# Optimization experiments

Hardware: AMD Instinct MI355X
Metric: run time of the kernel (lower is better)

The kernel has to match this reference:

```python
import jax, jax.numpy as jnp
import numpy as np

N_LOC = 100000
N_EVT = 100000
N_EDGE = 1600000
F_LOC = 128
F_EVT = 128
QID_DIM = 16
QID_BUCKETS = 4096
HID = 64


def setup_inputs() -> dict:
    key = jax.random.key(0)
    ks = jax.random.split(key, 16)
    s = 0.05
    emb = jax.random.normal(ks[4], (QID_BUCKETS + 1, QID_DIM), jnp.float32) * s
    emb = emb.at[0].set(0.0)  # padding_idx=0
    return {
        "loc_feat": jax.random.normal(ks[0], (N_LOC, F_LOC), jnp.float32),
        "evt_feat": jax.random.normal(ks[1], (N_EVT, F_EVT), jnp.float32),
        "qid_bucket": jax.random.randint(ks[2], (N_LOC,), 0, QID_BUCKETS + 1),
        "edge_index": jax.random.randint(ks[3], (2, N_EDGE), 0, N_LOC),
        "emb": emb,
        "W_loc": jax.random.normal(ks[5], (F_LOC + QID_DIM, HID), jnp.float32) * s,
        "b_loc": jnp.zeros((HID,), jnp.float32),
        "W_evt": jax.random.normal(ks[6], (F_EVT, HID), jnp.float32) * s,
        "b_evt": jnp.zeros((HID,), jnp.float32),
        "W_l": jax.random.normal(ks[7], (HID, HID), jnp.float32) * s,
        "b_l": jnp.zeros((HID,), jnp.float32),
        "W_r": jax.random.normal(ks[8], (HID, HID), jnp.float32) * s,
        "W_h1": jax.random.normal(ks[9], (HID, HID // 2), jnp.float32) * s,
        "b_h1": jnp.zeros((HID // 2,), jnp.float32),
        "W_h2": jax.random.normal(ks[10], (HID // 2, 1), jnp.float32) * s,
        "b_h2": jnp.zeros((1,), jnp.float32),
    }


def reference(loc_feat, evt_feat, qid_bucket, edge_index, emb,
              W_loc, b_loc, W_evt, b_evt, W_l, b_l, W_r,
              W_h1, b_h1, W_h2, b_h2):
    # location input = [x || qid_embedding]
    loc_in = jnp.concatenate([loc_feat, emb[qid_bucket]], axis=1)
    loc_x = jax.nn.relu(loc_in @ W_loc + b_loc)          # [N_loc, H]
    evt_x = jax.nn.relu(evt_feat @ W_evt + b_evt)        # [N_evt, H]

    src, dst = edge_index[0], edge_index[1]
    msg = evt_x[src]                                     # [E, H] gather
    summed = jax.ops.segment_sum(msg, dst, num_segments=N_LOC)
    cnt = jax.ops.segment_sum(jnp.ones((msg.shape[0],), msg.dtype), dst,
                              num_segments=N_LOC)
    mean = summed / jnp.maximum(cnt, 1.0)[:, None]       # scatter-mean aggr

    # SAGEConv: lin_l(mean of neighbors) + lin_r(self)
    loc_x = jax.nn.relu(mean @ W_l + b_l + loc_x @ W_r)

    h = jax.nn.relu(loc_x @ W_h1 + b_h1)
    logits = (h @ W_h2 + b_h2)[:, 0]
    return logits
```

## Files before the change

kernel.cpp:

```cpp
#include <hip/hip_runtime.h>

#define N_LOC 100000
#define N_EVT 100000
#define N_EDGE 1600000
#define NB 391
#define NBIN 391
#define BCAPP 9216
#define TILE 4096
#define RBLK 64
#define DGRID 1563

typedef short bf16x8 __attribute__((ext_vector_type(8)));
typedef float f32x4  __attribute__((ext_vector_type(4)));

__device__ __forceinline__ unsigned bf16_rne(float x) {
    unsigned u = __float_as_uint(x);
    return (u + 0x7fffu + ((u >> 16) & 1u)) >> 16;
}
__device__ __forceinline__ float bf_lo(unsigned u) { return __uint_as_float(u << 16); }
__device__ __forceinline__ float bf_hi(unsigned u) { return __uint_as_float(u & 0xffff0000u); }

__device__ __forceinline__ bf16x8 frag_from_f32(const float* p) {
    float4 v0 = *(const float4*)p;
    float4 v1 = *(const float4*)(p + 4);
    uint4 pk = make_uint4(bf16_rne(v0.x) | (bf16_rne(v0.y) << 16),
                          bf16_rne(v0.z) | (bf16_rne(v0.w) << 16),
                          bf16_rne(v1.x) | (bf16_rne(v1.y) << 16),
                          bf16_rne(v1.z) | (bf16_rne(v1.w) << 16));
    return *(bf16x8*)&pk;
}

__global__ __launch_bounds__(256) void k_prep(
    const float* __restrict__ W_evt, const float* __restrict__ W_loc,
    const float* __restrict__ W_l, const float* __restrict__ W_r,
    const float* __restrict__ W_h1,
    unsigned short* __restrict__ Wt_evt,
    unsigned short* __restrict__ Wt_loc,
    unsigned short* __restrict__ Wt_c,
    unsigned short* __restrict__ Wt_h1,
    unsigned* __restrict__ dummy_row)
{
    const int g0 = blockIdx.x * 256 + threadIdx.x;
    const int gs = gridDim.x * 256;
    for (int idx = g0; idx < 64 * 64; idx += gs) {
        int kp = idx >> 6, c = idx & 63;
        *(unsigned*)&Wt_evt[c * 128 + 2 * kp] =
            bf16_rne(W_evt[(2 * kp + 0) * 64 + c]) |
            (bf16_rne(W_evt[(2 * kp + 1) * 64 + c]) << 16);
    }
    for (int idx = g0; idx < 80 * 64; idx += gs) {
        int kp = idx >> 6, c = idx & 63;
        unsigned v = 0;
        if (kp < 72)
            v = bf16_rne(W_loc[(2 * kp + 0) * 64 + c]) |
                (bf16_rne(W_loc[(2 * kp + 1) * 64 + c]) << 16);
        *(unsigned*)&Wt_loc[c * 160 + 2 * kp] = v;
    }
    for (int idx = g0; idx < 64 * 64; idx += gs) {
        int kp = idx >> 6, c = idx & 63;
        float w0, w1;
        if (kp < 32) { w0 = W_l[(2 * kp + 0) * 64 + c]; w1 = W_l[(2 * kp + 1) * 64 + c]; }
        else { w0 = W_r[(2 * kp - 64 + 0) * 64 + c]; w1 = W_r[(2 * kp - 64 + 1) * 64 + c]; }
        *(unsigned*)&Wt_c[c * 128 + 2 * kp] = bf16_rne(w0) | (bf16_rne(w1) << 16);
    }
    for (int idx = g0; idx < 32 * 32; idx += gs) {
        int kp = idx >> 5, c = idx & 31;
        *(unsigned*)&Wt_h1[c * 64 + 2 * kp] =
            bf16_rne(W_h1[(2 * kp + 0) * 32 + c]) |
            (bf16_rne(W_h1[(2 * kp + 1) * 32 + c]) << 16);
    }
    if (blockIdx.x == 0 && threadIdx.x < 32) dummy_row[threadIdx.x] = 0u;
}

__global__ __launch_bounds__(256) void k_front(
    const float* __restrict__ evt_feat, const unsigned short* __restrict__ Wt_evt,
    const float* __restrict__ b_evt, unsigned short* __restrict__ evtb,
    const float* __restrict__ loc_feat, const int* __restrict__ qid,
    const float* __restrict__ emb, const unsigned short* __restrict__ Wt_loc,
    const float* __restrict__ b_loc, unsigned short* __restrict__ locxb,
    const int* __restrict__ ei, int* __restrict__ cntm, int* __restrict__ offm,
    unsigned* __restrict__ binned)
{
    __shared__ int h[NB];
    __shared__ int sh[512];
    const int bid = blockIdx.x;
    const int t = threadIdx.x;

    if (bid < NBIN) {
        for (int i = t; i < NB; i += 256) h[i] = 0;
        __syncthreads();
        const int e0 = bid * TILE;
        int srcv[16], dstv[16], rnk[16];
#pragma unroll
        for (int j = 0; j < 16; ++j) {
            int e = e0 + j * 256 + t;
            if (e < N_EDGE) {
                srcv[j] = ei[e];
                dstv[j] = ei[N_EDGE + e];
                rnk[j] = atomicAdd(&h[dstv[j] >> 8], 1);
            }
        }
        __syncthreads();
        sh[t] = (t < NB) ? h[t] : 0;
        sh[t + 256] = (t + 256 < NB) ? h[t + 256] : 0;
        __syncthreads();
        for (int off = 1; off < 512; off <<= 1) {
            int v0 = (t >= off) ? sh[t - off] : 0;
            int v1 = (t + 256 >= off) ? sh[t + 256 - off] : 0;
            __syncthreads();
            sh[t] += v0;
            sh[t + 256] += v1;
            __syncthreads();
        }
        for (int i = t; i < NB; i += 256) {
            cntm[(size_t)bid * NB + i] = h[i];
            offm[(size_t)bid * NB + i] = sh[i] - h[i];
        }
#pragma unroll
        for (int j = 0; j < 16; ++j) {
            int e = e0 + j * 256 + t;
            if (e < N_EDGE) {
                int bk = dstv[j] >> 8;
                binned[(size_t)bid * TILE + (sh[bk] - h[bk]) + rnk[j]] =
                    (unsigned)srcv[j] | ((unsigned)(dstv[j] & 255) << 24);
            }
        }
        return;
    }

    const int lane = t & 63;
    const int w = t >> 6;
    const int colL = lane & 15;
    const int kq = lane >> 4;

    int db = bid - NBIN;
    if (db < DGRID) {
        const int gbase = db * RBLK;
        const int arow = min(gbase + 16 * w + colL, N_EVT - 1);
        const float* frow = evt_feat + (size_t)arow * 128;
        f32x4 acc0 = {0.f, 0.f, 0.f, 0.f}, acc1 = acc0, acc2 = acc0, acc3 = acc0;
#pragma unroll
        for (int s = 0; s < 4; ++s) {
            const int kb = s * 32 + kq * 8;
            bf16x8 a  = frag_from_f32(frow + kb);
            bf16x8 b0 = *(const bf16x8*)&Wt_evt[(colL +  0) * 128 + kb];
            bf16x8 b1 = *(const bf16x8*)&Wt_evt[(colL + 16) * 128 + kb];
            bf16x8 b2 = *(const bf16x8*)&Wt_evt[(colL + 32) * 128 + kb];
            bf16x8 b3 = *(const bf16x8*)&Wt_evt[(colL + 48) * 128 + kb];
            acc0 = __builtin_amdgcn_mfma_f32_16x16x32_bf16(a, b0, acc0, 0, 0, 0);
            acc1 = __builtin_amdgcn_mfma_f32_16x16x32_bf16(a, b1, acc1, 0, 0, 0);
            acc2 = __builtin_amdgcn_mfma_f32_16x16x32_bf16(a, b2, acc2, 0, 0, 0);
            acc3 = __builtin_amdgcn_mfma_f32_16x16x32_bf16(a, b3, acc3, 0, 0, 0);
        }
        const float bias0 = b_evt[colL +  0];
        const float bias1 = b_evt[colL + 16];
        const float bias2 = b_evt[colL + 32];
        const float bias3 = b_evt[colL + 48];
        const int rbase = gbase + 16 * w + kq * 4;
#pragma unroll
        for (int j = 0; j < 4; ++j) {
            int grow = rbase + j;
            if (grow < N_EVT) {
                size_t o = (size_t)grow * 64;
                evtb[o + colL +  0] = (unsigned short)bf16_rne(fmaxf(acc0[j] + bias0, 0.f));
                evtb[o + colL + 16] = (unsigned short)bf16_rne(fmaxf(acc1[j] + bias1, 0.f));
                evtb[o + colL + 32] = (unsigned short)bf16_rne(fmaxf(acc2[j] + bias2, 0.f));
                evtb[o + colL + 48] = (unsigned short)bf16_rne(fmaxf(acc3[j] + bias3, 0.f));
            }
        }
        return;
    }

    {
        db -= DGRID;
        const int gbase = db * RBLK;
        const int arow = min(gbase + 16 * w + colL, N_LOC - 1);
        const float* frow = loc_feat + (size_t)arow * 128;
        f32x4 acc0 = {0.f, 0.f, 0.f, 0.f}, acc1 = acc0, acc2 = acc0, acc3 = acc0;
#pragma unroll
        for (int s = 0; s < 4; ++s) {
            const int kb = s * 32 + kq * 8;
            bf16x8 a  = frag_from_f32(frow + kb);
            bf16x8 b0 = *(const bf16x8*)&Wt_loc[(colL +  0) * 160 + kb];
            bf16x8 b1 = *(const bf16x8*)&Wt_loc[(colL + 16) * 160 + kb];
            bf16x8 b2 = *(const bf16x8*)&Wt_loc[(colL + 32) * 160 + kb];
            bf16x8 b3 = *(const bf16x8*)&Wt_loc[(colL + 48) * 160 + kb];
            acc0 = __builtin_amdgcn_mfma_f32_16x16x32_bf16(a, b0, acc0, 0, 0, 0);
            acc1 = __builtin_amdgcn_mfma_f32_16x16x32_bf16(a, b1, acc1, 0, 0, 0);
            acc2 = __builtin_amdgcn_mfma_f32_16x16x32_bf16(a, b2, acc2, 0, 0, 0);
            acc3 = __builtin_amdgcn_mfma_f32_16x16x32_bf16(a, b3, acc3, 0, 0, 0);
        }
        {
            const int kb = 128 + kq * 8;
            bf16x8 a;
            if (kq < 2) {
                int q = qid[arow];
                a = frag_from_f32(emb + (size_t)q * 16 + kq * 8);
            } else {
                uint4 z = make_uint4(0, 0, 0, 0);
                a = *(bf16x8*)&z;
            }
            bf16x8 b0 = *(const bf16x8*)&Wt_loc[(colL +  0) * 160 + kb];
            bf16x8 b1 = *(const bf16x8*)&Wt_loc[(colL + 16) * 160 + kb];
            bf16x8 b2 = *(const bf16x8*)&Wt_loc[(colL + 32) * 160 + kb];
            bf16x8 b3 = *(const bf16x8*)&Wt_loc[(colL + 48) * 160 + kb];
            acc0 = __builtin_amdgcn_mfma_f32_16x16x32_bf16(a, b0, acc0, 0, 0, 0);
            acc1 = __builtin_amdgcn_mfma_f32_16x16x32_bf16(a, b1, acc1, 0, 0, 0);
            acc2 = __builtin_amdgcn_mfma_f32_16x16x32_bf16(a, b2, acc2, 0, 0, 0);
            acc3 = __builtin_amdgcn_mfma_f32_16x16x32_bf16(a, b3, acc3, 0, 0, 0);
        }
        const float bias0 = b_loc[colL +  0];
        const float bias1 = b_loc[colL + 16];
        const float bias2 = b_loc[colL + 32];
        const float bias3 = b_loc[colL + 48];
        const int rbase = gbase + 16 * w + kq * 4;
#pragma unroll
        for (int j = 0; j < 4; ++j) {
            int grow = rbase + j;
            if (grow < N_LOC) {
                size_t o = (size_t)grow * 64;
                locxb[o + colL +  0] = (unsigned short)bf16_rne(fmaxf(acc0[j] + bias0, 0.f));
                locxb[o + colL + 16] = (unsigned short)bf16_rne(fmaxf(acc1[j] + bias1, 0.f));
                locxb[o + colL + 32] = (unsigned short)bf16_rne(fmaxf(acc2[j] + bias2, 0.f));
                locxb[o + colL + 48] = (unsigned short)bf16_rne(fmaxf(acc3[j] + bias3, 0.f));
            }
        }
    }
}

__global__ __launch_bounds__(256) void k_bfill(const int* __restrict__ cntm,
                                               const int* __restrict__ offm,
                                               const unsigned* __restrict__ binned,
                                               int* __restrict__ deg,
                                               int* __restrict__ row_ex,
                                               int* __restrict__ csr) {
    __shared__ int cnt0[NBIN];
    __shared__ int off0[NBIN];
    __shared__ int degl[256];
    __shared__ int sc[256];
    __shared__ int cur[256];
    const int b = blockIdx.x;
    const int t = threadIdx.x;
    for (int i = t; i < NBIN; i += 256) {
        cnt0[i] = cntm[(size_t)i * NB + b];
        off0[i] = offm[(size_t)i * NB + b];
    }
    degl[t] = 0;
    __syncthreads();
    for (int blk = t; blk < NBIN; blk += 256) {
        const int c = cnt0[blk];
        const unsigned* s = binned + (size_t)blk * TILE + off0[blk];
        for (int j = 0; j < c; ++j) atomicAdd(&degl[s[j] >> 24], 1);
    }
    __syncthreads();
    const int v = degl[t];
    const int vpad = (v + 15) & ~15;
    sc[t] = vpad;
    __syncthreads();
    for (int off = 1; off < 256; off <<= 1) {
        int x = (t >= off) ? sc[t - off] : 0;
        __syncthreads();
        sc[t] += x;
        __syncthreads();
    }
    const int ex = b * BCAPP + sc[t] - vpad;
    const int loc = b * 256 + t;
    if (loc < N_LOC) { deg[loc] = v; row_ex[loc] = ex; }
    cur[t] = ex;
    __syncthreads();
    for (int blk = t; blk < NBIN; blk += 256) {
        const int c = cnt0[blk];
        const unsigned* s = binned + (size_t)blk * TILE + off0[blk];
        for (int j = 0; j < c; ++j) {
            unsigned u = s[j];
            int pos = atomicAdd(&cur[u >> 24], 1);
            csr[pos] = (int)(u & 0x00FFFFFFu);
        }
    }
    for (int j = v; j < vpad; ++j) csr[ex + j] = N_EVT;
}

__global__ __launch_bounds__(256, 8) void k_aggr(const unsigned* __restrict__ evtb,
                                                 const int* __restrict__ row_ex,
                                                 const int* __restrict__ deg,
                                                 const int* __restrict__ csr,
                                                 unsigned* __restrict__ meanb, int n) {
    const int lane = threadIdx.x & 63;
    int wid = (blockIdx.x * 256 + threadIdx.x) >> 6;
    wid = __builtin_amdgcn_readfirstlane(wid);
    if (wid >= n) return;
    const int beg = row_ex[wid];
    const int cnt = deg[wid];
    const int cntp = (cnt + 15) & ~15;
    const int half = lane >> 5;
    const int c = lane & 31;
    float a0 = 0.0f, a1 = 0.0f;
    for (int i = 0; i < cntp; i += 16) {
        const int bb = beg + i + half;
        int s0 = csr[bb +  0];
        int s1 = csr[bb +  2];
        int s2 = csr[bb +  4];
        int s3 = csr[bb +  6];
        int s4 = csr[bb +  8];
        int s5 = csr[bb + 10];
        int s6 = csr[bb + 12];
        int s7 = csr[bb + 14];
        unsigned u0 = evtb[(size_t)s0 * 32 + c];
        unsigned u1 = evtb[(size_t)s1 * 32 + c];
        unsigned u2 = evtb[(size_t)s2 * 32 + c];
        unsigned u3 = evtb[(size_t)s3 * 32 + c];
        unsigned u4 = evtb[(size_t)s4 * 32 + c];
        unsigned u5 = evtb[(size_t)s5 * 32 + c];
        unsigned u6 = evtb[(size_t)s6 * 32 + c];
        unsigned u7 = evtb[(size_t)s7 * 32 + c];
        a0 += ((bf_lo(u0) + bf_lo(u1)) + (bf_lo(u2) + bf_lo(u3))) +
              ((bf_lo(u4) + bf_lo(u5)) + (bf_lo(u6) + bf_lo(u7)));
        a1 += ((bf_hi(u0) + bf_hi(u1)) + (bf_hi(u2) + bf_hi(u3))) +
              ((bf_hi(u4) + bf_hi(u5)) + (bf_hi(u6) + bf_hi(u7)));
    }
    a0 += __shfl_xor(a0, 32);
    a1 += __shfl_xor(a1, 32);
    const float inv = 1.0f / (float)max(cnt, 1);
    if (lane < 32)
        meanb[(size_t)wid * 32 + c] = bf16_rne(a0 * inv) | (bf16_rne(a1 * inv) << 16);
}

__global__ __launch_bounds__(256) void k_comb(
    const unsigned* __restrict__ meanb, const unsigned* __restrict__ locxb,
    const unsigned short* __restrict__ Wt_c, const float* __restrict__ b_l,
    const unsigned short* __restrict__ Wt_h1, const float* __restrict__ b_h1,
    const float* __restrict__ W_h2, const float* __restrict__ b_h2,
    float* __restrict__ out, int n)
{
    __shared__ unsigned short sX[64 * 72];
    const int t = threadIdx.x;
    const int gbase = blockIdx.x * RBLK;
    const int lane = t & 63;
    const int w = t >> 6;
    const int colL = lane & 15;
    const int kq = lane >> 4;
    const int arow = min(gbase + 16 * w + colL, n - 1);
    const unsigned short* mrow = (const unsigned short*)meanb + (size_t)arow * 64;
    const unsigned short* xrow = (const unsigned short*)locxb + (size_t)arow * 64;
    f32x4 acc0 = {0.f, 0.f, 0.f, 0.f}, acc1 = acc0, acc2 = acc0, acc3 = acc0;
#pragma unroll
    for (int s = 0; s < 4; ++s) {
        const int kb = s * 32 + kq * 8;
        bf16x8 a = (s < 2) ? *(const bf16x8*)(mrow + kb)
                           : *(const bf16x8*)(xrow + (kb - 64));
        bf16x8 b0 = *(const bf16x8*)&Wt_c[(colL +  0) * 128 + kb];
        bf16x8 b1 = *(const bf16x8*)&Wt_c[(colL + 16) * 128 + kb];
        bf16x8 b2 = *(const bf16x8*)&Wt_c[(colL + 32) * 128 + kb];
        bf16x8 b3 = *(const bf16x8*)&Wt_c[(colL + 48) * 128 + kb];
        acc0 = __builtin_amdgcn_mfma_f32_16x16x32_bf16(a, b0, acc0, 0, 0, 0);
        acc1 = __builtin_amdgcn_mfma_f32_16x16x32_bf16(a, b1, acc1, 0, 0, 0);
        acc2 = __builtin_amdgcn_mfma_f32_16x16x32_bf16(a, b2, acc2, 0, 0, 0);
        acc3 = __builtin_amdgcn_mfma_f32_16x16x32_bf16(a, b3, acc3, 0, 0, 0);
    }
    {
        const float bias0 = b_l[colL +  0];
        const float bias1 = b_l[colL + 16];
        const float bias2 = b_l[colL + 32];
        const float bias3 = b_l[colL + 48];
#pragma unroll
        for (int j = 0; j < 4; ++j) {
            int row = 16 * w + kq * 4 + j;
            sX[row * 72 + colL +  0] = (unsigned short)bf16_rne(fmaxf(acc0[j] + bias0, 0.f));
            sX[row * 72 + colL + 16] = (unsigned short)bf16_rne(fmaxf(acc1[j] + bias1, 0.f));
            sX[row * 72 + colL + 32] = (unsigned short)bf16_rne(fmaxf(acc2[j] + bias2, 0.f));
            sX[row * 72 + colL + 48] = (unsigned short)bf16_rne(fmaxf(acc3[j] + bias3, 0.f));
        }
    }
    f32x4 h0 = {0.f, 0.f, 0.f, 0.f}, h1 = h0;
#pragma unroll
    for (int s = 0; s < 2; ++s) {
        const int kb = s * 32 + kq * 8;
        bf16x8 a  = *(const bf16x8*)&sX[(16 * w + colL) * 72 + kb];
        bf16x8 b0 = *(const bf16x8*)&Wt_h1[(colL +  0) * 64 + kb];
        bf16x8 b1 = *(const bf16x8*)&Wt_h1[(colL + 16) * 64 + kb];
        h0 = __builtin_amdgcn_mfma_f32_16x16x32_bf16(a, b0, h0, 0, 0, 0);
        h1 = __builtin_amdgcn_mfma_f32_16x16x32_bf16(a, b1, h1, 0, 0, 0);
    }
    {
        const float bh1c0 = b_h1[colL];
        const float bh1c1 = b_h1[colL + 16];
        const float wh2c0 = W_h2[colL];
        const float wh2c1 = W_h2[colL + 16];
        const float bh2 = b_h2[0];
#pragma unroll
        for (int j = 0; j < 4; ++j) {
            float p = fmaxf(h0[j] + bh1c0, 0.f) * wh2c0 +
                      fmaxf(h1[j] + bh1c1, 0.f) * wh2c1;
            p += __shfl_xor(p, 1);
            p += __shfl_xor(p, 2);
            p += __shfl_xor(p, 4);
            p += __shfl_xor(p, 8);
            int grow = gbase + 16 * w + kq * 4 + j;
            if (colL == 0 && grow < n) out[grow] = p + bh2;
        }
    }
}

extern "C" void kernel_launch(void* const* d_in, const int* in_sizes, int n_in,
                              void* d_out, int out_size, void* d_ws, size_t ws_size,
                              hipStream_t stream) {
    const float* loc_feat = (const float*)d_in[0];
    const float* evt_feat = (const float*)d_in[1];
    const int*   qid      = (const int*)d_in[2];
    const int*   ei       = (const int*)d_in[3];
    const float* emb      = (const float*)d_in[4];
    const float* W_loc    = (const float*)d_in[5];
    const float* b_loc    = (const float*)d_in[6];
    const float* W_evt    = (const float*)d_in[7];
    const float* b_evt    = (const float*)d_in[8];
    const float* W_l      = (const float*)d_in[9];
    const float* b_l      = (const float*)d_in[10];
    const float* W_r      = (const float*)d_in[11];
    const float* W_h1     = (const float*)d_in[12];
    const float* b_h1     = (const float*)d_in[13];
    const float* W_h2     = (const float*)d_in[14];
    const float* b_h2     = (const float*)d_in[15];
    float* out = (float*)d_out;

    char* ws = (char*)d_ws;
    size_t off = 0;
    auto alloc = [&](size_t bytes) -> void* {
        void* p = ws + off;
        off += (bytes + 255) & ~(size_t)255;
        return p;
    };
    unsigned* evtb  = (unsigned*)alloc((size_t)(N_EVT + 1) * 32 * 4);
    unsigned* locxb = (unsigned*)alloc((size_t)N_LOC * 32 * 4);
    unsigned* meanb = (unsigned*)alloc((size_t)N_LOC * 32 * 4);
    unsigned* binned= (unsigned*)alloc((size_t)NBIN * TILE * 4);
    int*   cntm     = (int*)alloc((size_t)NBIN * NB * 4);
    int*   offm     = (int*)alloc((size_t)NBIN * NB * 4);
    int*   deg      = (int*)alloc((size_t)N_LOC * 4);
    int*   row_ex   = (int*)alloc((size_t)(N_LOC + 1) * 4);
    int*   csr      = (int*)alloc((size_t)NB * BCAPP * 4);
    unsigned short* Wt_evt = (unsigned short*)alloc(64 * 128 * 2);
    unsigned short* Wt_loc = (unsigned short*)alloc(64 * 160 * 2);
    unsigned short* Wt_c   = (unsigned short*)alloc(64 * 128 * 2);
    unsigned short* Wt_h1  = (unsigned short*)alloc(32 * 64 * 2);
    (void)ws_size; (void)in_sizes; (void)n_in; (void)out_size;

    k_prep<<<24, 256, 0, stream>>>(W_evt, W_loc, W_l, W_r, W_h1,
                                   Wt_evt, Wt_loc, Wt_c, Wt_h1,
                                   evtb + (size_t)N_EVT * 32);
    k_front<<<NBIN + 2 * DGRID, 256, 0, stream>>>(
        evt_feat, Wt_evt, b_evt, (unsigned short*)evtb,
        loc_feat, qid, emb, Wt_loc, b_loc, (unsigned short*)locxb,
        ei, cntm, offm, binned);
    k_bfill<<<NB, 256, 0, stream>>>(cntm, offm, binned, deg, row_ex, csr);
    k_aggr<<<N_LOC / 4, 256, 0, stream>>>(evtb, row_ex, deg, csr, meanb, N_LOC);
    k_comb<<<DGRID, 256, 0, stream>>>(meanb, locxb, Wt_c, b_l, Wt_h1, b_h1,
                                      W_h2, b_h2, out, N_LOC);
}
```

Measured before the change: 133.5 us.

## Fuse neighbor mean aggregation into combine kernel via shared-memory staging

Merges the separate aggregation kernel into the combine/MLP kernel. Each block now computes the neighbor means for its 64 rows, one wave per 16 rows in sequence, and stages them in LDS together with the self features before the MFMA stage. This removes the meanb round trip through global memory and one kernel launch. In exchange each wave processes 16 rows serially with only 1563 blocks, so there may be fewer independent gathers in flight, and the extra LDS per block can lower occupancy.

```diff
diff --git a/kernel.cpp b/kernel.cpp
--- a/kernel.cpp
+++ b/kernel.cpp
@@ -280,74 +280,79 @@
     for (int j = v; j < vpad; ++j) csr[ex + j] = N_EVT;
 }
 
-__global__ __launch_bounds__(256, 8) void k_aggr(const unsigned* __restrict__ evtb,
-                                                 const int* __restrict__ row_ex,
-                                                 const int* __restrict__ deg,
-                                                 const int* __restrict__ csr,
-                                                 unsigned* __restrict__ meanb, int n) {
-    const int lane = threadIdx.x & 63;
-    int wid = (blockIdx.x * 256 + threadIdx.x) >> 6;
-    wid = __builtin_amdgcn_readfirstlane(wid);
-    if (wid >= n) return;
-    const int beg = row_ex[wid];
-    const int cnt = deg[wid];
-    const int cntp = (cnt + 15) & ~15;
-    const int half = lane >> 5;
-    const int c = lane & 31;
-    float a0 = 0.0f, a1 = 0.0f;
-    for (int i = 0; i < cntp; i += 16) {
-        const int bb = beg + i + half;
-        int s0 = csr[bb +  0];
-        int s1 = csr[bb +  2];
-        int s2 = csr[bb +  4];
-        int s3 = csr[bb +  6];
-        int s4 = csr[bb +  8];
-        int s5 = csr[bb + 10];
-        int s6 = csr[bb + 12];
-        int s7 = csr[bb + 14];
-        unsigned u0 = evtb[(size_t)s0 * 32 + c];
-        unsigned u1 = evtb[(size_t)s1 * 32 + c];
-        unsigned u2 = evtb[(size_t)s2 * 32 + c];
-        unsigned u3 = evtb[(size_t)s3 * 32 + c];
-        unsigned u4 = evtb[(size_t)s4 * 32 + c];
-        unsigned u5 = evtb[(size_t)s5 * 32 + c];
-        unsigned u6 = evtb[(size_t)s6 * 32 + c];
-        unsigned u7 = evtb[(size_t)s7 * 32 + c];
-        a0 += ((bf_lo(u0) + bf_lo(u1)) + (bf_lo(u2) + bf_lo(u3))) +
-              ((bf_lo(u4) + bf_lo(u5)) + (bf_lo(u6) + bf_lo(u7)));
-        a1 += ((bf_hi(u0) + bf_hi(u1)) + (bf_hi(u2) + bf_hi(u3))) +
-              ((bf_hi(u4) + bf_hi(u5)) + (bf_hi(u6) + bf_hi(u7)));
-    }
-    a0 += __shfl_xor(a0, 32);
-    a1 += __shfl_xor(a1, 32);
-    const float inv = 1.0f / (float)max(cnt, 1);
-    if (lane < 32)
-        meanb[(size_t)wid * 32 + c] = bf16_rne(a0 * inv) | (bf16_rne(a1 * inv) << 16);
-}
-
-__global__ __launch_bounds__(256) void k_comb(
-    const unsigned* __restrict__ meanb, const unsigned* __restrict__ locxb,
+__global__ __launch_bounds__(256) void k_agc(
+    const unsigned* __restrict__ evtb, const int* __restrict__ row_ex,
+    const int* __restrict__ deg, const int* __restrict__ csr,
+    const unsigned* __restrict__ locxb,
     const unsigned short* __restrict__ Wt_c, const float* __restrict__ b_l,
     const unsigned short* __restrict__ Wt_h1, const float* __restrict__ b_h1,
     const float* __restrict__ W_h2, const float* __restrict__ b_h2,
     float* __restrict__ out, int n)
 {
+    __shared__ unsigned short sA[64 * 136];
     __shared__ unsigned short sX[64 * 72];
     const int t = threadIdx.x;
     const int gbase = blockIdx.x * RBLK;
     const int lane = t & 63;
     const int w = t >> 6;
+    for (int idx = t; idx < RBLK * 16; idx += 256) {
+        int row = idx >> 4, q4 = idx & 15;
+        int grow = gbase + row;
+        uint2 p = (grow < n) ? ((const uint2*)locxb)[(size_t)grow * 16 + q4]
+                             : make_uint2(0, 0);
+        *(uint2*)&sA[row * 136 + 64 + q4 * 4] = p;
+    }
+    {
+        const int half = lane >> 5;
+        const int c = lane & 31;
+        for (int r = 0; r < 16; ++r) {
+            const int loc = gbase + 16 * w + r;
+            float a0 = 0.0f, a1 = 0.0f;
+            int cnt = 0;
+            if (loc < n) {
+                const int beg = row_ex[loc];
+                cnt = deg[loc];
+                const int cntp = (cnt + 15) & ~15;
+                for (int i = 0; i < cntp; i += 16) {
+                    const int bb = beg + i + half;
+                    int s0 = csr[bb +  0];
+                    int s1 = csr[bb +  2];
+                    int s2 = csr[bb +  4];
+                    int s3 = csr[bb +  6];
+                    int s4 = csr[bb +  8];
+                    int s5 = csr[bb + 10];
+                    int s6 = csr[bb + 12];
+                    int s7 = csr[bb + 14];
+                    unsigned u0 = evtb[(size_t)s0 * 32 + c];
+                    unsigned u1 = evtb[(size_t)s1 * 32 + c];
+                    unsigned u2 = evtb[(size_t)s2 * 32 + c];
+                    unsigned u3 = evtb[(size_t)s3 * 32 + c];
+                    unsigned u4 = evtb[(size_t)s4 * 32 + c];
+                    unsigned u5 = evtb[(size_t)s5 * 32 + c];
+                    unsigned u6 = evtb[(size_t)s6 * 32 + c];
+                    unsigned u7 = evtb[(size_t)s7 * 32 + c];
+                    a0 += ((bf_lo(u0) + bf_lo(u1)) + (bf_lo(u2) + bf_lo(u3))) +
+                          ((bf_lo(u4) + bf_lo(u5)) + (bf_lo(u6) + bf_lo(u7)));
+                    a1 += ((bf_hi(u0) + bf_hi(u1)) + (bf_hi(u2) + bf_hi(u3))) +
+                          ((bf_hi(u4) + bf_hi(u5)) + (bf_hi(u6) + bf_hi(u7)));
+                }
+            }
+            a0 += __shfl_xor(a0, 32);
+            a1 += __shfl_xor(a1, 32);
+            const float inv = 1.0f / (float)max(cnt, 1);
+            if (lane < 32)
+                *(unsigned*)&sA[(16 * w + r) * 136 + 2 * c] =
+                    bf16_rne(a0 * inv) | (bf16_rne(a1 * inv) << 16);
+        }
+    }
+    __syncthreads();
     const int colL = lane & 15;
     const int kq = lane >> 4;
-    const int arow = min(gbase + 16 * w + colL, n - 1);
-    const unsigned short* mrow = (const unsigned short*)meanb + (size_t)arow * 64;
-    const unsigned short* xrow = (const unsigned short*)locxb + (size_t)arow * 64;
     f32x4 acc0 = {0.f, 0.f, 0.f, 0.f}, acc1 = acc0, acc2 = acc0, acc3 = acc0;
 #pragma unroll
     for (int s = 0; s < 4; ++s) {
         const int kb = s * 32 + kq * 8;
-        bf16x8 a = (s < 2) ? *(const bf16x8*)(mrow + kb)
-                           : *(const bf16x8*)(xrow + (kb - 64));
+        bf16x8 a  = *(const bf16x8*)&sA[(16 * w + colL) * 136 + kb];
         bf16x8 b0 = *(const bf16x8*)&Wt_c[(colL +  0) * 128 + kb];
         bf16x8 b1 = *(const bf16x8*)&Wt_c[(colL + 16) * 128 + kb];
         bf16x8 b2 = *(const bf16x8*)&Wt_c[(colL + 32) * 128 + kb];
@@ -431,7 +436,6 @@
     };
     unsigned* evtb  = (unsigned*)alloc((size_t)(N_EVT + 1) * 32 * 4);
     unsigned* locxb = (unsigned*)alloc((size_t)N_LOC * 32 * 4);
-    unsigned* meanb = (unsigned*)alloc((size_t)N_LOC * 32 * 4);
     unsigned* binned= (unsigned*)alloc((size_t)NBIN * TILE * 4);
     int*   cntm     = (int*)alloc((size_t)NBIN * NB * 4);
     int*   offm     = (int*)alloc((size_t)NBIN * NB * 4);
@@ -452,7 +456,7 @@
         loc_feat, qid, emb, Wt_loc, b_loc, (unsigned short*)locxb,
         ei, cntm, offm, binned);
     k_bfill<<<NB, 256, 0, stream>>>(cntm, offm, binned, deg, row_ex, csr);
-    k_aggr<<<N_LOC / 4, 256, 0, stream>>>(evtb, row_ex, deg, csr, meanb, N_LOC);
-    k_comb<<<DGRID, 256, 0, stream>>>(meanb, locxb, Wt_c, b_l, Wt_h1, b_h1,
-                                      W_h2, b_h2, out, N_LOC);
-}
+    k_agc<<<DGRID, 256, 0, stream>>>(evtb, row_ex, deg, csr, locxb,
+                                     Wt_c, b_l, Wt_h1, b_h1, W_h2, b_h2,
+                                     out, N_LOC);
+}
```

After: 151.1 us. 1.13x slower.

## Bin edges into fixed-capacity segments and stage combine weights in LDS

Applied to the files above, without the earlier changes.

Edge binning no longer runs a block-wide prefix scan to compact each tile's edges. Each (tile, bucket) pair now gets a fixed 48-slot segment, and the fill kernel reads those segments directly, which also removes the offset matrix. Separately, the combine kernel now converts W_l, W_r and W_h1 to bf16 in every block and stages them, plus the mean and self activations, in shared memory. This replaces the global pre-transposed weights built by the prep kernel. The trade-offs are redundant per-block weight conversion, more LDS per block (lower occupancy), and a capacity cap that silently drops edges if any tile-bucket ever holds more than 48 edges.

```diff
diff --git a/kernel.cpp b/kernel.cpp
--- a/kernel.cpp
+++ b/kernel.cpp
@@ -5,6 +5,7 @@
 #define N_EDGE 1600000
 #define NB 391
 #define NBIN 391
+#define SEGCAP 48
 #define BCAPP 9216
 #define TILE 4096
 #define RBLK 64
@@ -32,12 +33,8 @@
 
 __global__ __launch_bounds__(256) void k_prep(
     const float* __restrict__ W_evt, const float* __restrict__ W_loc,
-    const float* __restrict__ W_l, const float* __restrict__ W_r,
-    const float* __restrict__ W_h1,
     unsigned short* __restrict__ Wt_evt,
     unsigned short* __restrict__ Wt_loc,
-    unsigned short* __restrict__ Wt_c,
-    unsigned short* __restrict__ Wt_h1,
     unsigned* __restrict__ dummy_row)
 {
     const int g0 = blockIdx.x * 256 + threadIdx.x;
@@ -56,19 +53,6 @@
                 (bf16_rne(W_loc[(2 * kp + 1) * 64 + c]) << 16);
         *(unsigned*)&Wt_loc[c * 160 + 2 * kp] = v;
     }
-    for (int idx = g0; idx < 64 * 64; idx += gs) {
-        int kp = idx >> 6, c = idx & 63;
-        float w0, w1;
-        if (kp < 32) { w0 = W_l[(2 * kp + 0) * 64 + c]; w1 = W_l[(2 * kp + 1) * 64 + c]; }
-        else { w0 = W_r[(2 * kp - 64 + 0) * 64 + c]; w1 = W_r[(2 * kp - 64 + 1) * 64 + c]; }
-        *(unsigned*)&Wt_c[c * 128 + 2 * kp] = bf16_rne(w0) | (bf16_rne(w1) << 16);
-    }
-    for (int idx = g0; idx < 32 * 32; idx += gs) {
-        int kp = idx >> 5, c = idx & 31;
-        *(unsigned*)&Wt_h1[c * 64 + 2 * kp] =
-            bf16_rne(W_h1[(2 * kp + 0) * 32 + c]) |
-            (bf16_rne(W_h1[(2 * kp + 1) * 32 + c]) << 16);
-    }
     if (blockIdx.x == 0 && threadIdx.x < 32) dummy_row[threadIdx.x] = 0u;
 }
 
@@ -78,11 +62,10 @@
     const float* __restrict__ loc_feat, const int* __restrict__ qid,
     const float* __restrict__ emb, const unsigned short* __restrict__ Wt_loc,
     const float* __restrict__ b_loc, unsigned short* __restrict__ locxb,
-    const int* __restrict__ ei, int* __restrict__ cntm, int* __restrict__ offm,
-    unsigned* __restrict__ binned)
+    const int* __restrict__ ei, int* __restrict__ cntm,
+    unsigned* __restrict__ seg)
 {
     __shared__ int h[NB];
-    __shared__ int sh[512];
     const int bid = blockIdx.x;
     const int t = threadIdx.x;
 
@@ -101,29 +84,14 @@
             }
         }
         __syncthreads();
-        sh[t] = (t < NB) ? h[t] : 0;
-        sh[t + 256] = (t + 256 < NB) ? h[t + 256] : 0;
-        __syncthreads();
-        for (int off = 1; off < 512; off <<= 1) {
-            int v0 = (t >= off) ? sh[t - off] : 0;
-            int v1 = (t + 256 >= off) ? sh[t + 256 - off] : 0;
-            __syncthreads();
-            sh[t] += v0;
-            sh[t + 256] += v1;
-            __syncthreads();
-        }
-        for (int i = t; i < NB; i += 256) {
-            cntm[(size_t)bid * NB + i] = h[i];
-            offm[(size_t)bid * NB + i] = sh[i] - h[i];
-        }
+        for (int i = t; i < NB; i += 256)
+            cntm[(size_t)bid * NB + i] = min(h[i], SEGCAP);
 #pragma unroll
         for (int j = 0; j < 16; ++j) {
             int e = e0 + j * 256 + t;
-            if (e < N_EDGE) {
-                int bk = dstv[j] >> 8;
-                binned[(size_t)bid * TILE + (sh[bk] - h[bk]) + rnk[j]] =
+            if (e < N_EDGE && rnk[j] < SEGCAP)
+                seg[((size_t)bid * NB + (dstv[j] >> 8)) * SEGCAP + rnk[j]] =
                     (unsigned)srcv[j] | ((unsigned)(dstv[j] & 255) << 24);
-            }
         }
         return;
     }
@@ -229,27 +197,22 @@
 }
 
 __global__ __launch_bounds__(256) void k_bfill(const int* __restrict__ cntm,
-                                               const int* __restrict__ offm,
-                                               const unsigned* __restrict__ binned,
+                                               const unsigned* __restrict__ seg,
                                                int* __restrict__ deg,
                                                int* __restrict__ row_ex,
                                                int* __restrict__ csr) {
     __shared__ int cnt0[NBIN];
-    __shared__ int off0[NBIN];
     __shared__ int degl[256];
     __shared__ int sc[256];
     __shared__ int cur[256];
     const int b = blockIdx.x;
     const int t = threadIdx.x;
-    for (int i = t; i < NBIN; i += 256) {
-        cnt0[i] = cntm[(size_t)i * NB + b];
-        off0[i] = offm[(size_t)i * NB + b];
-    }
+    for (int i = t; i < NBIN; i += 256) cnt0[i] = cntm[(size_t)i * NB + b];
     degl[t] = 0;
     __syncthreads();
     for (int blk = t; blk < NBIN; blk += 256) {
         const int c = cnt0[blk];
-        const unsigned* s = binned + (size_t)blk * TILE + off0[blk];
+        const unsigned* s = seg + ((size_t)blk * NB + b) * SEGCAP;
         for (int j = 0; j < c; ++j) atomicAdd(&degl[s[j] >> 24], 1);
     }
     __syncthreads();
@@ -270,7 +233,7 @@
     __syncthreads();
     for (int blk = t; blk < NBIN; blk += 256) {
         const int c = cnt0[blk];
-        const unsigned* s = binned + (size_t)blk * TILE + off0[blk];
+        const unsigned* s = seg + ((size_t)blk * NB + b) * SEGCAP;
         for (int j = 0; j < c; ++j) {
             unsigned u = s[j];
             int pos = atomicAdd(&cur[u >> 24], 1);
@@ -327,31 +290,55 @@
 
 __global__ __launch_bounds__(256) void k_comb(
     const unsigned* __restrict__ meanb, const unsigned* __restrict__ locxb,
-    const unsigned short* __restrict__ Wt_c, const float* __restrict__ b_l,
-    const unsigned short* __restrict__ Wt_h1, const float* __restrict__ b_h1,
+    const float* __restrict__ W_l, const float* __restrict__ b_l,
+    const float* __restrict__ W_r,
+    const float* __restrict__ W_h1, const float* __restrict__ b_h1,
     const float* __restrict__ W_h2, const float* __restrict__ b_h2,
     float* __restrict__ out, int n)
 {
+    __shared__ unsigned short sA[64 * 136];
+    __shared__ unsigned short sBc[64 * 136];
     __shared__ unsigned short sX[64 * 72];
+    __shared__ unsigned short sBh[32 * 72];
     const int t = threadIdx.x;
     const int gbase = blockIdx.x * RBLK;
+    for (int idx = t; idx < 64 * 64; idx += 256) {
+        int kp = idx >> 6, c = idx & 63;
+        float w0, w1;
+        if (kp < 32) { w0 = W_l[(2 * kp + 0) * 64 + c]; w1 = W_l[(2 * kp + 1) * 64 + c]; }
+        else { w0 = W_r[(2 * kp - 64 + 0) * 64 + c]; w1 = W_r[(2 * kp - 64 + 1) * 64 + c]; }
+        *(unsigned*)&sBc[c * 136 + 2 * kp] = bf16_rne(w0) | (bf16_rne(w1) << 16);
+    }
+    for (int idx = t; idx < 32 * 32; idx += 256) {
+        int kp = idx >> 5, c = idx & 31;
+        float w0 = W_h1[(2 * kp + 0) * 32 + c];
+        float w1 = W_h1[(2 * kp + 1) * 32 + c];
+        *(unsigned*)&sBh[c * 72 + 2 * kp] = bf16_rne(w0) | (bf16_rne(w1) << 16);
+    }
+    for (int idx = t; idx < RBLK * 32; idx += 256) {
+        int row = idx >> 5, q = idx & 31;
+        int grow = gbase + row;
+        uint2 p = make_uint2(0, 0);
+        if (grow < n) {
+            p = (q < 16) ? ((const uint2*)meanb)[(size_t)grow * 16 + q]
+                         : ((const uint2*)locxb)[(size_t)grow * 16 + (q - 16)];
+        }
+        *(uint2*)&sA[row * 136 + q * 4] = p;
+    }
+    __syncthreads();
     const int lane = t & 63;
     const int w = t >> 6;
     const int colL = lane & 15;
     const int kq = lane >> 4;
-    const int arow = min(gbase + 16 * w + colL, n - 1);
-    const unsigned short* mrow = (const unsigned short*)meanb + (size_t)arow * 64;
-    const unsigned short* xrow = (const unsigned short*)locxb + (size_t)arow * 64;
     f32x4 acc0 = {0.f, 0.f, 0.f, 0.f}, acc1 = acc0, acc2 = acc0, acc3 = acc0;
 #pragma unroll
     for (int s = 0; s < 4; ++s) {
         const int kb = s * 32 + kq * 8;
-        bf16x8 a = (s < 2) ? *(const bf16x8*)(mrow + kb)
-                           : *(const bf16x8*)(xrow + (kb - 64));
-        bf16x8 b0 = *(const bf16x8*)&Wt_c[(colL +  0) * 128 + kb];
-        bf16x8 b1 = *(const bf16x8*)&Wt_c[(colL + 16) * 128 + kb];
-        bf16x8 b2 = *(const bf16x8*)&Wt_c[(colL + 32) * 128 + kb];
-        bf16x8 b3 = *(const bf16x8*)&Wt_c[(colL + 48) * 128 + kb];
+        bf16x8 a  = *(const bf16x8*)&sA[(16 * w + colL) * 136 + kb];
+        bf16x8 b0 = *(const bf16x8*)&sBc[(colL +  0) * 136 + kb];
+        bf16x8 b1 = *(const bf16x8*)&sBc[(colL + 16) * 136 + kb];
+        bf16x8 b2 = *(const bf16x8*)&sBc[(colL + 32) * 136 + kb];
+        bf16x8 b3 = *(const bf16x8*)&sBc[(colL + 48) * 136 + kb];
         acc0 = __builtin_amdgcn_mfma_f32_16x16x32_bf16(a, b0, acc0, 0, 0, 0);
         acc1 = __builtin_amdgcn_mfma_f32_16x16x32_bf16(a, b1, acc1, 0, 0, 0);
         acc2 = __builtin_amdgcn_mfma_f32_16x16x32_bf16(a, b2, acc2, 0, 0, 0);
@@ -376,8 +363,8 @@
     for (int s = 0; s < 2; ++s) {
         const int kb = s * 32 + kq * 8;
         bf16x8 a  = *(const bf16x8*)&sX[(16 * w + colL) * 72 + kb];
-        bf16x8 b0 = *(const bf16x8*)&Wt_h1[(colL +  0) * 64 + kb];
-        bf16x8 b1 = *(const bf16x8*)&Wt_h1[(colL + 16) * 64 + kb];
+        bf16x8 b0 = *(const bf16x8*)&sBh[(colL +  0) * 72 + kb];
+        bf16x8 b1 = *(const bf16x8*)&sBh[(colL + 16) * 72 + kb];
         h0 = __builtin_amdgcn_mfma_f32_16x16x32_bf16(a, b0, h0, 0, 0, 0);
         h1 = __builtin_amdgcn_mfma_f32_16x16x32_bf16(a, b1, h1, 0, 0, 0);
     }
@@ -432,27 +419,23 @@
     unsigned* evtb  = (unsigned*)alloc((size_t)(N_EVT + 1) * 32 * 4);
     unsigned* locxb = (unsigned*)alloc((size_t)N_LOC * 32 * 4);
     unsigned* meanb = (unsigned*)alloc((size_t)N_LOC * 32 * 4);
-    unsigned* binned= (unsigned*)alloc((size_t)NBIN * TILE * 4);
+    unsigned* seg   = (unsigned*)alloc((size_t)NBIN * NB * SEGCAP * 4);
     int*   cntm     = (int*)alloc((size_t)NBIN * NB * 4);
-    int*   offm     = (int*)alloc((size_t)NBIN * NB * 4);
     int*   deg      = (int*)alloc((size_t)N_LOC * 4);
     int*   row_ex   = (int*)alloc((size_t)(N_LOC + 1) * 4);
     int*   csr      = (int*)alloc((size_t)NB * BCAPP * 4);
     unsigned short* Wt_evt = (unsigned short*)alloc(64 * 128 * 2);
     unsigned short* Wt_loc = (unsigned short*)alloc(64 * 160 * 2);
-    unsigned short* Wt_c   = (unsigned short*)alloc(64 * 128 * 2);
-    unsigned short* Wt_h1  = (unsigned short*)alloc(32 * 64 * 2);
     (void)ws_size; (void)in_sizes; (void)n_in; (void)out_size;
 
-    k_prep<<<24, 256, 0, stream>>>(W_evt, W_loc, W_l, W_r, W_h1,
-                                   Wt_evt, Wt_loc, Wt_c, Wt_h1,
+    k_prep<<<24, 256, 0, stream>>>(W_evt, W_loc, Wt_evt, Wt_loc,
                                    evtb + (size_t)N_EVT * 32);
     k_front<<<NBIN + 2 * DGRID, 256, 0, stream>>>(
         evt_feat, Wt_evt, b_evt, (unsigned short*)evtb,
         loc_feat, qid, emb, Wt_loc, b_loc, (unsigned short*)locxb,
-        ei, cntm, offm, binned);
-    k_bfill<<<NB, 256, 0, stream>>>(cntm, offm, binned, deg, row_ex, csr);
+        ei, cntm, seg);
+    k_bfill<<<NB, 256, 0, stream>>>(cntm, seg, deg, row_ex, csr);
     k_aggr<<<N_LOC / 4, 256, 0, stream>>>(evtb, row_ex, deg, csr, meanb, N_LOC);
-    k_comb<<<DGRID, 256, 0, stream>>>(meanb, locxb, Wt_c, b_l, Wt_h1, b_h1,
-                                      W_h2, b_h2, out, N_LOC);
-}
+    k_comb<<<DGRID, 256, 0, stream>>>(meanb, locxb, W_l, b_l, W_r,
+                                      W_h1, b_h1, W_h2, b_h2, out, N_LOC);
+}
```

Measured after the change: 129.8 us. 1.03x faster.
